# Performance work log

Hardware: AMD Instinct MI355X
Metric: run time of the kernel (lower is better)

The kernel has to match this reference:

```python
import jax, jax.numpy as jnp
import numpy as np

N_NODES = 100000
N_EDGES = 1600000
DIM = 64
NEG_SLOPE = 0.2  # DGL GATConv default
BN_EPS = 1e-5


def setup_inputs() -> dict:
    key = jax.random.key(0)
    ks = jax.random.split(key, 16)
    d = {}
    d["node_weight"] = jax.random.normal(ks[0], (N_NODES, DIM), jnp.float32)
    d["edge_weight"] = jax.random.normal(ks[1], (N_EDGES,), jnp.float32)  # unused in forward (faithful to source)
    d["src"] = jax.random.randint(ks[2], (N_EDGES,), 0, N_NODES)
    d["dst"] = jax.random.randint(ks[3], (N_EDGES,), 0, N_NODES)
    i = 4
    scale = 1.0 / np.sqrt(DIM)
    for l in (1, 2, 3):
        d[f"W{l}"] = jax.random.normal(ks[i], (DIM, DIM), jnp.float32) * scale; i += 1
        d[f"al{l}"] = jax.random.normal(ks[i], (DIM,), jnp.float32) * 0.1; i += 1
        d[f"ar{l}"] = jax.random.normal(ks[i], (DIM,), jnp.float32) * 0.1; i += 1
        d[f"b{l}"] = jnp.zeros((DIM,), jnp.float32)
        d[f"g{l}"] = jnp.ones((DIM,), jnp.float32)
        d[f"beta{l}"] = jnp.zeros((DIM,), jnp.float32)
    return d


def gat_layer(h, src, dst, W, al, ar, b):
    # DGL GATConv, 1 head: project, edge attention, per-dst softmax, scatter-add
    feat = h @ W                                  # [N, D]
    el = feat @ al                                # [N]
    er = feat @ ar                                # [N]
    e = jax.nn.leaky_relu(el[src] + er[dst], NEG_SLOPE)   # [E]
    m = jax.ops.segment_max(e, dst, num_segments=N_NODES)  # per-dst max
    ex = jnp.exp(e - m[dst])
    s = jax.ops.segment_sum(ex, dst, num_segments=N_NODES)
    alpha = ex / s[dst]                           # edge softmax
    out = jax.ops.segment_sum(alpha[:, None] * feat[src], dst, num_segments=N_NODES)
    return out + b


def batchnorm(h, g, beta):
    # BatchNorm1d in training mode: batch stats, biased variance
    mu = jnp.mean(h, axis=0)
    var = jnp.mean(jnp.square(h - mu), axis=0)
    return (h - mu) * jax.lax.rsqrt(var + BN_EPS) * g + beta


def reference(node_weight, edge_weight, src, dst,
              W1, al1, ar1, b1, g1, beta1,
              W2, al2, ar2, b2, g2, beta2,
              W3, al3, ar3, b3, g3, beta3):
    # dropout is identity in eval mode
    h = gat_layer(node_weight, src, dst, W1, al1, ar1, b1)
    h = jax.nn.elu(batchnorm(h, g1, beta1))
    h = gat_layer(h, src, dst, W2, al2, ar2, b2)
    h = jax.nn.elu(batchnorm(h, g2, beta2))
    h = gat_layer(h, src, dst, W3, al3, ar3, b3)
    h = batchnorm(h, g3, beta3)
    return h
```

## Files before the change

kernel.cpp:

```cpp
#include <hip/hip_runtime.h>
#include <hip/hip_bf16.h>
#include <math.h>

#define DIM 64
#define BSHIFT 9
#define BNODES 512
#define MAXB 256
#define EPT 8
#define CHUNK 2048

typedef __attribute__((ext_vector_type(8))) short bf16x8;
typedef __attribute__((ext_vector_type(4))) float f32x4;

__device__ __forceinline__ short f2bf(float x) {
    union { __hip_bfloat16 b; short s; } u;
    u.b = __float2bfloat16(x);
    return u.s;
}
__device__ __forceinline__ float bf2f(short s) {
    return __uint_as_float(((unsigned)(unsigned short)s) << 16);
}


__global__ void bin_count_kernel(const int* __restrict__ dst, int* __restrict__ bucket_cnt, int E) {
    __shared__ int h[MAXB];
    int t = threadIdx.x;
    h[t] = 0;
    __syncthreads();
    for (int i = blockIdx.x * blockDim.x + t; i < E; i += gridDim.x * blockDim.x)
        atomicAdd(&h[dst[i] >> BSHIFT], 1);
    __syncthreads();
    if (h[t]) atomicAdd(&bucket_cnt[t], h[t]);
}

__global__ void bucket_scan_kernel(const int* __restrict__ bucket_cnt,
                                   int* __restrict__ bucket_off, int* __restrict__ bucket_fill) {
    __shared__ int s[MAXB];
    int t = threadIdx.x;
    int v = bucket_cnt[t];
    s[t] = v;
    __syncthreads();
    for (int off = 1; off < MAXB; off <<= 1) {
        int x = (t >= off) ? s[t - off] : 0;
        __syncthreads();
        s[t] += x;
        __syncthreads();
    }
    bucket_off[t] = s[t] - v;
    bucket_fill[t] = 0;
}

__global__ __launch_bounds__(256) void bin_scatter_kernel(
    const int* __restrict__ src, const int* __restrict__ dst,
    const int* __restrict__ bucket_off, int* __restrict__ bucket_fill,
    unsigned long long* __restrict__ binned, int E) {
    __shared__ int lcnt[MAXB];
    __shared__ int lbase[MAXB];
    int t = threadIdx.x;
    lcnt[t] = 0;
    __syncthreads();
    int base = blockIdx.x * CHUNK;
    unsigned long long pair[EPT];
    int slot[EPT];
#pragma unroll
    for (int j = 0; j < EPT; j++) {
        int idx = base + j * 256 + t;
        if (idx < E) {
            int s = src[idx], d = dst[idx];
            pair[j] = ((unsigned long long)(unsigned)d << 32) | (unsigned)s;
            slot[j] = atomicAdd(&lcnt[d >> BSHIFT], 1);
        } else {
            slot[j] = -1;
        }
    }
    __syncthreads();
    int c = lcnt[t];
    if (c) lbase[t] = atomicAdd(&bucket_fill[t], c);
    __syncthreads();
#pragma unroll
    for (int j = 0; j < EPT; j++) {
        if (slot[j] >= 0) {
            int b = (int)(pair[j] >> 32) >> BSHIFT;
            binned[(size_t)bucket_off[b] + lbase[b] + slot[j]] = pair[j];
        }
    }
}

__global__ __launch_bounds__(256) void node_count_kernel(
    const unsigned long long* __restrict__ binned, const int* __restrict__ bucket_off,
    const int* __restrict__ bucket_cnt, int* __restrict__ counts, int N) {
    __shared__ int cnt[BNODES];
    int b = blockIdx.x, t = threadIdx.x;
    for (int i = t; i < BNODES; i += 256) cnt[i] = 0;
    __syncthreads();
    int s0 = bucket_off[b], c = bucket_cnt[b];
    for (int i = t; i < c; i += 256) {
        int d = (int)(binned[(size_t)s0 + i] >> 32);
        atomicAdd(&cnt[d & (BNODES - 1)], 1);
    }
    __syncthreads();
    int nbase = b << BSHIFT;
    for (int i = t; i < BNODES; i += 256)
        if (nbase + i < N) counts[nbase + i] = cnt[i];
}

__global__ void scan1_kernel(const int* __restrict__ counts, int* __restrict__ excl,
                             int* __restrict__ blk_sums, int n) {
    __shared__ int sdata[256];
    int t = threadIdx.x;
    int base = blockIdx.x * 1024 + t * 4;
    int v0 = (base + 0 < n) ? counts[base + 0] : 0;
    int v1 = (base + 1 < n) ? counts[base + 1] : 0;
    int v2 = (base + 2 < n) ? counts[base + 2] : 0;
    int v3 = (base + 3 < n) ? counts[base + 3] : 0;
    int tsum = v0 + v1 + v2 + v3;
    sdata[t] = tsum;
    __syncthreads();
    for (int off = 1; off < 256; off <<= 1) {
        int x = (t >= off) ? sdata[t - off] : 0;
        __syncthreads();
        sdata[t] += x;
        __syncthreads();
    }
    int run = sdata[t] - tsum;
    if (base + 0 < n) excl[base + 0] = run; run += v0;
    if (base + 1 < n) excl[base + 1] = run; run += v1;
    if (base + 2 < n) excl[base + 2] = run; run += v2;
    if (base + 3 < n) excl[base + 3] = run;
    if (t == 255) blk_sums[blockIdx.x] = sdata[255];
}

__global__ void scan2_kernel(int* __restrict__ blk_sums, int nb) {
    __shared__ int s[128];
    int t = threadIdx.x;
    s[t] = (t < nb) ? blk_sums[t] : 0;
    __syncthreads();
    for (int off = 1; off < 128; off <<= 1) {
        int x = (t >= off) ? s[t - off] : 0;
        __syncthreads();
        s[t] += x;
        __syncthreads();
    }
    if (t < nb) blk_sums[t] = (t > 0) ? s[t - 1] : 0;
}

__global__ void scan3_kernel(int* __restrict__ excl, const int* __restrict__ blk_sums,
                             int n, int total) {
    int i = blockIdx.x * blockDim.x + threadIdx.x;
    if (i < n) excl[i] += blk_sums[i >> 10];
    if (i == 0) excl[n] = total;
}

__global__ __launch_bounds__(256) void final_scatter_kernel(
    const unsigned long long* __restrict__ binned, const int* __restrict__ bucket_off,
    const int* __restrict__ bucket_cnt, const int* __restrict__ row_ptr,
    int* __restrict__ src_sorted, int N) {
    __shared__ int fill[BNODES];
    int b = blockIdx.x, t = threadIdx.x;
    for (int i = t; i < BNODES; i += 256) fill[i] = 0;
    __syncthreads();
    int s0 = bucket_off[b], c = bucket_cnt[b];
    for (int i = t; i < c; i += 256) {
        unsigned long long p = binned[(size_t)s0 + i];
        int d = (int)(p >> 32);
        int pos = row_ptr[d] + atomicAdd(&fill[d & (BNODES - 1)], 1);
        src_sorted[pos] = (int)(p & 0xffffffffu);
    }
}


__global__ void wlr_kernel(
    const float* __restrict__ W1, const float* __restrict__ al1, const float* __restrict__ ar1,
    const float* __restrict__ W2, const float* __restrict__ al2, const float* __restrict__ ar2,
    const float* __restrict__ W3, const float* __restrict__ al3, const float* __restrict__ ar3,
    float* __restrict__ wlr, short* __restrict__ wfrag) {
    const float* W  = (blockIdx.x == 0) ? W1  : (blockIdx.x == 1) ? W2  : W3;
    const float* al = (blockIdx.x == 0) ? al1 : (blockIdx.x == 1) ? al2 : al3;
    const float* ar = (blockIdx.x == 0) ? ar1 : (blockIdx.x == 1) ? ar2 : ar3;
    int t = threadIdx.x;
    short* whi = wfrag + blockIdx.x * 8192;
    short* wlo = whi + 4096;
    for (int idx = t; idx < 4096; idx += 256) {
        int j = idx & 7, li = (idx >> 3) & 15, quad = (idx >> 7) & 3;
        int nt = (idx >> 9) & 3, ks = idx >> 11;
        int k = ks * 32 + quad * 8 + j, nn = nt * 16 + li;
        float w = W[k * 64 + nn];
        short hi = f2bf(w);
        whi[idx] = hi;
        wlo[idx] = f2bf(w - bf2f(hi));
    }
    if (t < 64) {
        float l = 0.f, r = 0.f;
        for (int nn = 0; nn < 64; nn++) {
            float w = W[t * 64 + nn];
            l = fmaf(w, al[nn], l);
            r = fmaf(w, ar[nn], r);
        }
        const float LOG2E = 1.4426950408889634f;
        wlr[blockIdx.x * 128 + t] = l * LOG2E;
        wlr[blockIdx.x * 128 + 64 + t] = r * LOG2E;
    }
}

__global__ __launch_bounds__(256) void gemm64_mfma_kernel(
    const float* __restrict__ h, const short* __restrict__ wfrag_l,
    const float* __restrict__ wl, const float* __restrict__ wr,
    const float* __restrict__ stats, const float* __restrict__ g,
    const float* __restrict__ beta, int do_bn, float invN,
    __hip_bfloat16* __restrict__ feat, float* __restrict__ el, float* __restrict__ er,
    int n) {
    int t = threadIdx.x;
    int lane = t & 63;
    int li = lane & 15;
    int quad = lane >> 4;
    int wv = t >> 6;

    const short* whi = wfrag_l;
    const short* wlo = wfrag_l + 4096;
    bf16x8 b_hi[2][4], b_lo[2][4];
#pragma unroll
    for (int ks = 0; ks < 2; ks++)
#pragma unroll
        for (int nt = 0; nt < 4; nt++) {
            int base = (((ks * 4 + nt) * 4 + quad) * 16 + li) * 8;
            b_hi[ks][nt] = *(const bf16x8*)(whi + base);
            b_lo[ks][nt] = *(const bf16x8*)(wlo + base);
        }
    float wlv[2][8], wrv[2][8];
#pragma unroll
    for (int ks = 0; ks < 2; ks++)
#pragma unroll
        for (int j = 0; j < 8; j++) {
            wlv[ks][j] = wl[ks * 32 + quad * 8 + j];
            wrv[ks][j] = wr[ks * 32 + quad * 8 + j];
        }

    float sc[2][8], sh[2][8];
    if (do_bn) {
#pragma unroll
        for (int ks = 0; ks < 2; ks++)
#pragma unroll
            for (int j = 0; j < 8; j++) {
                int k = ks * 32 + quad * 8 + j;
                float mu = stats[k] * invN;
                float var = fmaf(-mu, mu, stats[64 + k] * invN);
                float inv = rsqrtf(var + 1e-5f) * g[k];
                sc[ks][j] = inv;
                sh[ks][j] = beta[k] - mu * inv;
            }
    }

    int ntiles = (n + 15) >> 4;
    for (int tile = blockIdx.x * 4 + wv; tile < ntiles; tile += gridDim.x * 4) {
        int m0 = tile << 4;
        int rrow = m0 + li;
        const float* rowp = h + (size_t)((rrow < n) ? rrow : (n - 1)) * 64;
        bf16x8 a_hi[2], a_lo[2];
        float elp = 0.f, erp = 0.f;
#pragma unroll
        for (int ks = 0; ks < 2; ks++) {
            float4 v0 = *(const float4*)(rowp + ks * 32 + quad * 8);
            float4 v1 = *(const float4*)(rowp + ks * 32 + quad * 8 + 4);
            float x[8] = {v0.x, v0.y, v0.z, v0.w, v1.x, v1.y, v1.z, v1.w};
#pragma unroll
            for (int j = 0; j < 8; j++) {
                float v = x[j];
                if (do_bn) {
                    v = fmaf(v, sc[ks][j], sh[ks][j]);
                    if (v < 0.f) v = expm1f(v);
                }
                elp = fmaf(v, wlv[ks][j], elp);
                erp = fmaf(v, wrv[ks][j], erp);
                short hi = f2bf(v);
                a_hi[ks][j] = hi;
                a_lo[ks][j] = f2bf(v - bf2f(hi));
            }
        }
        elp += __shfl_xor(elp, 16, 64);
        elp += __shfl_xor(elp, 32, 64);
        erp += __shfl_xor(erp, 16, 64);
        erp += __shfl_xor(erp, 32, 64);
        if (lane < 16 && m0 + li < n) {
            el[m0 + li] = elp;
            er[m0 + li] = erp;
        }
        f32x4 acc[4];
#pragma unroll
        for (int nt = 0; nt < 4; nt++) acc[nt] = (f32x4){0.f, 0.f, 0.f, 0.f};
#pragma unroll
        for (int ks = 0; ks < 2; ks++)
#pragma unroll
            for (int nt = 0; nt < 4; nt++) {
                acc[nt] = __builtin_amdgcn_mfma_f32_16x16x32_bf16(a_hi[ks], b_hi[ks][nt], acc[nt], 0, 0, 0);
                acc[nt] = __builtin_amdgcn_mfma_f32_16x16x32_bf16(a_lo[ks], b_hi[ks][nt], acc[nt], 0, 0, 0);
                acc[nt] = __builtin_amdgcn_mfma_f32_16x16x32_bf16(a_hi[ks], b_lo[ks][nt], acc[nt], 0, 0, 0);
            }
#pragma unroll
        for (int nt = 0; nt < 4; nt++)
#pragma unroll
            for (int reg = 0; reg < 4; reg++) {
                int wrow = m0 + quad * 4 + reg;
                if (wrow < n) {
                    union { __hip_bfloat16 b; short s; } u;
                    u.s = f2bf(acc[nt][reg]);
                    feat[(size_t)wrow * 64 + nt * 16 + li] = u.b;
                }
            }
    }
}

#define AGG_LOAD(P, ELV, POS)                                  \
    {                                                          \
        int idx = (POS) + q;                                   \
        bool v = idx < end;                                    \
        int idc = v ? idx : end - 1;                           \
        int sn = src_sorted[idc];                              \
        float ev = el[sn];                                     \
        ELV = v ? ev : -INFINITY;                              \
        P = featv[(size_t)sn * 8 + li];                        \
    }

#define AGG_CHUNK(P, ELV)                                      \
    {                                                          \
        float e = ELV + er_n;                                  \
        e = fmaxf(e, 0.2f * e);                                \
        float w = exp2f(e);                                    \
        s += w;                                                \
        a0 = fmaf(w, __uint_as_float(P.x << 16), a0);          \
        a1 = fmaf(w, __uint_as_float(P.x & 0xffff0000u), a1);  \
        a2 = fmaf(w, __uint_as_float(P.y << 16), a2);          \
        a3 = fmaf(w, __uint_as_float(P.y & 0xffff0000u), a3);  \
        a4 = fmaf(w, __uint_as_float(P.z << 16), a4);          \
        a5 = fmaf(w, __uint_as_float(P.z & 0xffff0000u), a5);  \
        a6 = fmaf(w, __uint_as_float(P.w << 16), a6);          \
        a7 = fmaf(w, __uint_as_float(P.w & 0xffff0000u), a7);  \
    }

__global__ __launch_bounds__(256) void attn_agg_kernel(
    const int* __restrict__ row_ptr, const int* __restrict__ src_sorted,
    const float* __restrict__ el, const float* __restrict__ er,
    const __hip_bfloat16* __restrict__ feat, const float* __restrict__ bias,
    float* __restrict__ out, int n) {
    int t = threadIdx.x, lane = t & 63;
    int q = lane >> 3;
    int li = lane & 7;
    int node0 = blockIdx.x * 16 + (t >> 6) * 4;
    const uint4* featv = (const uint4*)feat;

#pragma unroll
    for (int j = 0; j < 4; j++) {
        int node = node0 + j;
        if (node >= n) break;
        int start = row_ptr[node], end = row_ptr[node + 1];
        float er_n = er[node];

        float s = 0.f;
        float a0 = 0.f, a1 = 0.f, a2 = 0.f, a3 = 0.f;
        float a4 = 0.f, a5 = 0.f, a6 = 0.f, a7 = 0.f;

        uint4 pA = {0u, 0u, 0u, 0u}, pB = {0u, 0u, 0u, 0u};
        float elA = -INFINITY, elB = -INFINITY;
        if (start < end) AGG_LOAD(pA, elA, start)
        if (start + 8 < end) AGG_LOAD(pB, elB, start + 8)
        for (int i = start; i < end; i += 16) {
            AGG_CHUNK(pA, elA)
            if (i + 16 < end) AGG_LOAD(pA, elA, i + 16)
            if (i + 8 < end) {
                AGG_CHUNK(pB, elB)
                if (i + 24 < end) AGG_LOAD(pB, elB, i + 24)
            }
        }
        s += __shfl_xor(s, 8, 64);
        s += __shfl_xor(s, 16, 64);
        s += __shfl_xor(s, 32, 64);
        bool b0 = (q & 1) != 0;
        float t0 = __shfl_xor(a0, 8, 64), t1 = __shfl_xor(a1, 8, 64);
        float t2 = __shfl_xor(a2, 8, 64), t3 = __shfl_xor(a3, 8, 64);
        float t4 = __shfl_xor(a4, 8, 64), t5 = __shfl_xor(a5, 8, 64);
        float t6 = __shfl_xor(a6, 8, 64), t7 = __shfl_xor(a7, 8, 64);
        float x0 = b0 ? (a4 + t4) : (a0 + t0);
        float x1 = b0 ? (a5 + t5) : (a1 + t1);
        float y0 = b0 ? (a6 + t6) : (a2 + t2);
        float y1 = b0 ? (a7 + t7) : (a3 + t3);
        bool b1 = (q & 2) != 0;
        float u0 = __shfl_xor(x0, 16, 64), u1 = __shfl_xor(x1, 16, 64);
        float v0 = __shfl_xor(y0, 16, 64), v1 = __shfl_xor(y1, 16, 64);
        float z0 = b1 ? (y0 + v0) : (x0 + u0);
        float z1 = b1 ? (y1 + v1) : (x1 + u1);
        z0 += __shfl_xor(z0, 32, 64);
        z1 += __shfl_xor(z1, 32, 64);
        float val = ((q & 4) != 0) ? z1 : z0;
        int d = li * 8 + ((q & 1) << 2) + (q & 2) + ((q >> 2) & 1);
        float inv_s = (s > 0.f) ? 1.f / s : 0.f;
        out[(size_t)node * 64 + d] = fmaf(val, inv_s, bias[d]);
    }
}

__global__ __launch_bounds__(256) void bn_stats_kernel(const float* __restrict__ h,
                                                       float* __restrict__ stats, int n) {
    __shared__ float ls[256], lss[256];
    int t = threadIdx.x, lane = t & 63;
    int w = blockIdx.x * 4 + (t >> 6);
    int stride = gridDim.x * 4;
    float s = 0.f, ss = 0.f;
    for (int row = w; row < n; row += stride) {
        float v = h[(size_t)row * DIM + lane];
        s += v;
        ss = fmaf(v, v, ss);
    }
    ls[t] = s; lss[t] = ss;
    __syncthreads();
    if (t < 64) {
        float a = ls[t] + ls[t + 64] + ls[t + 128] + ls[t + 192];
        float b = lss[t] + lss[t + 64] + lss[t + 128] + lss[t + 192];
        atomicAdd(&stats[t], a);
        atomicAdd(&stats[64 + t], b);
    }
}

__global__ void bn_apply_kernel(float* __restrict__ h, const float* __restrict__ stats,
                                const float* __restrict__ g, const float* __restrict__ beta,
                                int n, int do_elu) {
    int i = blockIdx.x * blockDim.x + threadIdx.x;
    int total = n * DIM;
    int stride = gridDim.x * blockDim.x;
    float invN = 1.f / (float)n;
    for (; i < total; i += stride) {
        int c = i & 63;
        float mu = stats[c] * invN;
        float var = fmaf(-mu, mu, stats[DIM + c] * invN);
        float x = (h[i] - mu) * rsqrtf(var + 1e-5f) * g[c] + beta[c];
        if (do_elu && x < 0.f) x = expm1f(x);
        h[i] = x;
    }
}


extern "C" void kernel_launch(void* const* d_in, const int* in_sizes, int n_in,
                              void* d_out, int out_size, void* d_ws, size_t ws_size,
                              hipStream_t stream) {
    const float* nw = (const float*)d_in[0];
    const int* src = (const int*)d_in[2];
    const int* dst = (const int*)d_in[3];
    const int N = in_sizes[0] / DIM;
    const int E = in_sizes[2];
    const float invN = 1.f / (float)N;
    const int nbuck = (N + BNODES - 1) >> BSHIFT;

    char* ws = (char*)d_ws;
    size_t off = 0;
    auto alloc = [&](size_t bytes) -> void* {
        void* p = ws + off;
        off += (bytes + 255) & ~(size_t)255;
        return p;
    };
    int* counts       = (int*)alloc((size_t)N * 4);
    int* row_ptr      = (int*)alloc(((size_t)N + 1) * 4);
    int* blk_sums     = (int*)alloc(512);
    int* bucket_cnt   = (int*)alloc(MAXB * 4);
    int* bucket_off   = (int*)alloc(MAXB * 4);
    int* bucket_fill  = (int*)alloc(MAXB * 4);
    unsigned long long* binned = (unsigned long long*)alloc((size_t)E * 8);
    int* src_sorted   = (int*)alloc((size_t)E * 4);
    float* el         = (float*)alloc((size_t)N * 4);
    float* er         = (float*)alloc((size_t)N * 4);
    __hip_bfloat16* feat = (__hip_bfloat16*)alloc((size_t)N * DIM * 2);
    float* hbuf       = (float*)alloc((size_t)N * DIM * 4);
    float* stats      = (float*)alloc(3 * 512);
    float* wlr        = (float*)alloc(3 * 128 * 4);
    short* wfrag      = (short*)alloc(3 * 8192 * 2);

    int nb = (N + 1023) / 1024;
    int ntiles = (N + 15) >> 4;

    hipMemsetAsync(bucket_cnt, 0, MAXB * 4, stream);
    hipMemsetAsync(stats, 0, 3 * 512, stream);
    wlr_kernel<<<3, 256, 0, stream>>>(
        (const float*)d_in[4],  (const float*)d_in[5],  (const float*)d_in[6],
        (const float*)d_in[10], (const float*)d_in[11], (const float*)d_in[12],
        (const float*)d_in[16], (const float*)d_in[17], (const float*)d_in[18],
        wlr, wfrag);
    bin_count_kernel<<<256, 256, 0, stream>>>(dst, bucket_cnt, E);
    bucket_scan_kernel<<<1, MAXB, 0, stream>>>(bucket_cnt, bucket_off, bucket_fill);
    bin_scatter_kernel<<<(E + CHUNK - 1) / CHUNK, 256, 0, stream>>>(
        src, dst, bucket_off, bucket_fill, binned, E);
    node_count_kernel<<<nbuck, 256, 0, stream>>>(binned, bucket_off, bucket_cnt, counts, N);
    scan1_kernel<<<nb, 256, 0, stream>>>(counts, row_ptr, blk_sums, N);
    scan2_kernel<<<1, 128, 0, stream>>>(blk_sums, nb);
    scan3_kernel<<<(N + 255) / 256, 256, 0, stream>>>(row_ptr, blk_sums, N, E);
    final_scatter_kernel<<<nbuck, 256, 0, stream>>>(binned, bucket_off, bucket_cnt,
                                                    row_ptr, src_sorted, N);

    for (int l = 0; l < 3; l++) {
        const float* b    = (const float*)d_in[7 + 6 * l];
        const float* hin = (l == 0) ? nw : hbuf;
        float* hout = (l == 2) ? (float*)d_out : hbuf;
        float* stats_prev = (l == 0) ? stats : stats + (l - 1) * 128;
        float* stats_cur  = stats + l * 128;

        gemm64_mfma_kernel<<<(ntiles + 3) / 4, 256, 0, stream>>>(
            hin, wfrag + l * 8192,
            wlr + l * 128, wlr + l * 128 + 64,
            stats_prev,
            (l == 0) ? (const float*)d_in[8] : (const float*)d_in[8 + 6 * (l - 1)],
            (l == 0) ? (const float*)d_in[9] : (const float*)d_in[9 + 6 * (l - 1)],
            (l > 0) ? 1 : 0, invN,
            feat, el, er, N);
        attn_agg_kernel<<<(N + 15) / 16, 256, 0, stream>>>(row_ptr, src_sorted, el, er,
                                                           feat, b, hout, N);
        bn_stats_kernel<<<512, 256, 0, stream>>>(hout, stats_cur, N);
    }
    bn_apply_kernel<<<2048, 256, 0, stream>>>((float*)d_out, stats + 2 * 128,
                                              (const float*)d_in[8 + 12],
                                              (const float*)d_in[9 + 12],
                                              N, 0);
}
```

Measured before the change: 474.0 us.

## Replace two-level bucketed CSR build with direct global-atomic count and scatter

Replaces the bucket-binning CSR construction (bin count, bucket scan, bin scatter, per-bucket node count, final scatter) with a single global-atomic per-node count kernel and a single global-atomic scatter kernel. This cuts several kernel launches and the intermediate 8-byte binned edge array pass. In exchange it relies on 1.6M global atomics spread over 100K counters and on scattered writes, where the old scheme used LDS atomics and bucket-local writes. Edge order within each destination row also becomes nondeterministic.

```diff
diff --git a/kernel.cpp b/kernel.cpp
--- a/kernel.cpp
+++ b/kernel.cpp
@@ -3,11 +3,6 @@
 #include <math.h>
 
 #define DIM 64
-#define BSHIFT 9
-#define BNODES 512
-#define MAXB 256
-#define EPT 8
-#define CHUNK 2048
 
 typedef __attribute__((ext_vector_type(8))) short bf16x8;
 typedef __attribute__((ext_vector_type(4))) float f32x4;
@@ -22,86 +17,25 @@
 }
 
 
-__global__ void bin_count_kernel(const int* __restrict__ dst, int* __restrict__ bucket_cnt, int E) {
-    __shared__ int h[MAXB];
-    int t = threadIdx.x;
-    h[t] = 0;
-    __syncthreads();
-    for (int i = blockIdx.x * blockDim.x + t; i < E; i += gridDim.x * blockDim.x)
-        atomicAdd(&h[dst[i] >> BSHIFT], 1);
-    __syncthreads();
-    if (h[t]) atomicAdd(&bucket_cnt[t], h[t]);
-}
-
-__global__ void bucket_scan_kernel(const int* __restrict__ bucket_cnt,
-                                   int* __restrict__ bucket_off, int* __restrict__ bucket_fill) {
-    __shared__ int s[MAXB];
-    int t = threadIdx.x;
-    int v = bucket_cnt[t];
-    s[t] = v;
-    __syncthreads();
-    for (int off = 1; off < MAXB; off <<= 1) {
-        int x = (t >= off) ? s[t - off] : 0;
-        __syncthreads();
-        s[t] += x;
-        __syncthreads();
-    }
-    bucket_off[t] = s[t] - v;
-    bucket_fill[t] = 0;
-}
-
-__global__ __launch_bounds__(256) void bin_scatter_kernel(
+__global__ __launch_bounds__(256) void count_kernel(
+    const int* __restrict__ dst, int* __restrict__ counts, int E) {
+    int i = blockIdx.x * blockDim.x + threadIdx.x;
+    int stride = gridDim.x * blockDim.x;
+    for (; i < E; i += stride)
+        atomicAdd(&counts[dst[i]], 1);
+}
+
+__global__ __launch_bounds__(256) void scatter_kernel(
     const int* __restrict__ src, const int* __restrict__ dst,
-    const int* __restrict__ bucket_off, int* __restrict__ bucket_fill,
-    unsigned long long* __restrict__ binned, int E) {
-    __shared__ int lcnt[MAXB];
-    __shared__ int lbase[MAXB];
-    int t = threadIdx.x;
-    lcnt[t] = 0;
-    __syncthreads();
-    int base = blockIdx.x * CHUNK;
-    unsigned long long pair[EPT];
-    int slot[EPT];
-#pragma unroll
-    for (int j = 0; j < EPT; j++) {
-        int idx = base + j * 256 + t;
-        if (idx < E) {
-            int s = src[idx], d = dst[idx];
-            pair[j] = ((unsigned long long)(unsigned)d << 32) | (unsigned)s;
-            slot[j] = atomicAdd(&lcnt[d >> BSHIFT], 1);
-        } else {
-            slot[j] = -1;
-        }
-    }
-    __syncthreads();
-    int c = lcnt[t];
-    if (c) lbase[t] = atomicAdd(&bucket_fill[t], c);
-    __syncthreads();
-#pragma unroll
-    for (int j = 0; j < EPT; j++) {
-        if (slot[j] >= 0) {
-            int b = (int)(pair[j] >> 32) >> BSHIFT;
-            binned[(size_t)bucket_off[b] + lbase[b] + slot[j]] = pair[j];
-        }
-    }
-}
-
-__global__ __launch_bounds__(256) void node_count_kernel(
-    const unsigned long long* __restrict__ binned, const int* __restrict__ bucket_off,
-    const int* __restrict__ bucket_cnt, int* __restrict__ counts, int N) {
-    __shared__ int cnt[BNODES];
-    int b = blockIdx.x, t = threadIdx.x;
-    for (int i = t; i < BNODES; i += 256) cnt[i] = 0;
-    __syncthreads();
-    int s0 = bucket_off[b], c = bucket_cnt[b];
-    for (int i = t; i < c; i += 256) {
-        int d = (int)(binned[(size_t)s0 + i] >> 32);
-        atomicAdd(&cnt[d & (BNODES - 1)], 1);
-    }
-    __syncthreads();
-    int nbase = b << BSHIFT;
-    for (int i = t; i < BNODES; i += 256)
-        if (nbase + i < N) counts[nbase + i] = cnt[i];
+    const int* __restrict__ row_ptr, int* __restrict__ fill,
+    int* __restrict__ src_sorted, int E) {
+    int i = blockIdx.x * blockDim.x + threadIdx.x;
+    int stride = gridDim.x * blockDim.x;
+    for (; i < E; i += stride) {
+        int d = dst[i];
+        int pos = row_ptr[d] + atomicAdd(&fill[d], 1);
+        src_sorted[pos] = src[i];
+    }
 }
 
 __global__ void scan1_kernel(const int* __restrict__ counts, int* __restrict__ excl,
@@ -149,23 +83,6 @@
     int i = blockIdx.x * blockDim.x + threadIdx.x;
     if (i < n) excl[i] += blk_sums[i >> 10];
     if (i == 0) excl[n] = total;
-}
-
-__global__ __launch_bounds__(256) void final_scatter_kernel(
-    const unsigned long long* __restrict__ binned, const int* __restrict__ bucket_off,
-    const int* __restrict__ bucket_cnt, const int* __restrict__ row_ptr,
-    int* __restrict__ src_sorted, int N) {
-    __shared__ int fill[BNODES];
-    int b = blockIdx.x, t = threadIdx.x;
-    for (int i = t; i < BNODES; i += 256) fill[i] = 0;
-    __syncthreads();
-    int s0 = bucket_off[b], c = bucket_cnt[b];
-    for (int i = t; i < c; i += 256) {
-        unsigned long long p = binned[(size_t)s0 + i];
-        int d = (int)(p >> 32);
-        int pos = row_ptr[d] + atomicAdd(&fill[d & (BNODES - 1)], 1);
-        src_sorted[pos] = (int)(p & 0xffffffffu);
-    }
 }
 
 
@@ -445,7 +362,6 @@
     const int N = in_sizes[0] / DIM;
     const int E = in_sizes[2];
     const float invN = 1.f / (float)N;
-    const int nbuck = (N + BNODES - 1) >> BSHIFT;
 
     char* ws = (char*)d_ws;
     size_t off = 0;
@@ -454,13 +370,10 @@
         off += (bytes + 255) & ~(size_t)255;
         return p;
     };
-    int* counts       = (int*)alloc((size_t)N * 4);
+    int* counts       = (int*)alloc((size_t)N * 2 * 4);
+    int* fill         = counts + N;
     int* row_ptr      = (int*)alloc(((size_t)N + 1) * 4);
     int* blk_sums     = (int*)alloc(512);
-    int* bucket_cnt   = (int*)alloc(MAXB * 4);
-    int* bucket_off   = (int*)alloc(MAXB * 4);
-    int* bucket_fill  = (int*)alloc(MAXB * 4);
-    unsigned long long* binned = (unsigned long long*)alloc((size_t)E * 8);
     int* src_sorted   = (int*)alloc((size_t)E * 4);
     float* el         = (float*)alloc((size_t)N * 4);
     float* er         = (float*)alloc((size_t)N * 4);
@@ -473,23 +386,18 @@
     int nb = (N + 1023) / 1024;
     int ntiles = (N + 15) >> 4;
 
-    hipMemsetAsync(bucket_cnt, 0, MAXB * 4, stream);
+    hipMemsetAsync(counts, 0, (size_t)N * 2 * 4, stream);
     hipMemsetAsync(stats, 0, 3 * 512, stream);
     wlr_kernel<<<3, 256, 0, stream>>>(
         (const float*)d_in[4],  (const float*)d_in[5],  (const float*)d_in[6],
         (const float*)d_in[10], (const float*)d_in[11], (const float*)d_in[12],
         (const float*)d_in[16], (const float*)d_in[17], (const float*)d_in[18],
         wlr, wfrag);
-    bin_count_kernel<<<256, 256, 0, stream>>>(dst, bucket_cnt, E);
-    bucket_scan_kernel<<<1, MAXB, 0, stream>>>(bucket_cnt, bucket_off, bucket_fill);
-    bin_scatter_kernel<<<(E + CHUNK - 1) / CHUNK, 256, 0, stream>>>(
-        src, dst, bucket_off, bucket_fill, binned, E);
-    node_count_kernel<<<nbuck, 256, 0, stream>>>(binned, bucket_off, bucket_cnt, counts, N);
+    count_kernel<<<2048, 256, 0, stream>>>(dst, counts, E);
     scan1_kernel<<<nb, 256, 0, stream>>>(counts, row_ptr, blk_sums, N);
     scan2_kernel<<<1, 128, 0, stream>>>(blk_sums, nb);
     scan3_kernel<<<(N + 255) / 256, 256, 0, stream>>>(row_ptr, blk_sums, N, E);
-    final_scatter_kernel<<<nbuck, 256, 0, stream>>>(binned, bucket_off, bucket_cnt,
-                                                    row_ptr, src_sorted, N);
+    scatter_kernel<<<2048, 256, 0, stream>>>(src, dst, row_ptr, fill, src_sorted, E);
 
     for (int l = 0; l < 3; l++) {
         const float* b    = (const float*)d_in[7 + 6 * l];
```

Result: slower. 567.7 us (+19.8%).

## Fuse CSR build into one per-bucket kernel and store hidden activations in bf16

Applied to the files above, without the earlier changes.

Replaces the node-count, three-stage global scan and final scatter kernels with a single per-bucket kernel. It computes local counts, does a shared-memory exclusive scan offset by the bucket base, writes row_ptr and scatters src indices, which removes four launches and the counts round-trip. Intermediate layer outputs (hbuf) are now stored as bf16 instead of fp32, halving the write traffic in attn_agg and the read traffic in bn_stats and the next GEMM. The cost is lower precision for intermediate activations before batchnorm statistics.

```diff
diff --git a/kernel.cpp b/kernel.cpp
--- a/kernel.cpp
+++ b/kernel.cpp
@@ -86,85 +86,45 @@
     }
 }
 
-__global__ __launch_bounds__(256) void node_count_kernel(
+__global__ __launch_bounds__(256) void csr_finalize_kernel(
     const unsigned long long* __restrict__ binned, const int* __restrict__ bucket_off,
-    const int* __restrict__ bucket_cnt, int* __restrict__ counts, int N) {
+    const int* __restrict__ bucket_cnt, int* __restrict__ row_ptr,
+    int* __restrict__ src_sorted, int N, int E, int nbuck) {
     __shared__ int cnt[BNODES];
+    __shared__ int excl[BNODES];
+    __shared__ int ps[256];
     int b = blockIdx.x, t = threadIdx.x;
     for (int i = t; i < BNODES; i += 256) cnt[i] = 0;
     __syncthreads();
     int s0 = bucket_off[b], c = bucket_cnt[b];
-    for (int i = t; i < c; i += 256) {
-        int d = (int)(binned[(size_t)s0 + i] >> 32);
-        atomicAdd(&cnt[d & (BNODES - 1)], 1);
-    }
+    for (int i = t; i < c; i += 256)
+        atomicAdd(&cnt[(int)(binned[(size_t)s0 + i] >> 32) & (BNODES - 1)], 1);
+    __syncthreads();
+    int a0 = cnt[2 * t], a1 = cnt[2 * t + 1];
+    int pairsum = a0 + a1;
+    ps[t] = pairsum;
+    __syncthreads();
+    for (int off = 1; off < 256; off <<= 1) {
+        int x = (t >= off) ? ps[t - off] : 0;
+        __syncthreads();
+        ps[t] += x;
+        __syncthreads();
+    }
+    int run = ps[t] - pairsum;
+    excl[2 * t] = run;
+    excl[2 * t + 1] = run + a0;
     __syncthreads();
     int nbase = b << BSHIFT;
     for (int i = t; i < BNODES; i += 256)
-        if (nbase + i < N) counts[nbase + i] = cnt[i];
-}
-
-__global__ void scan1_kernel(const int* __restrict__ counts, int* __restrict__ excl,
-                             int* __restrict__ blk_sums, int n) {
-    __shared__ int sdata[256];
-    int t = threadIdx.x;
-    int base = blockIdx.x * 1024 + t * 4;
-    int v0 = (base + 0 < n) ? counts[base + 0] : 0;
-    int v1 = (base + 1 < n) ? counts[base + 1] : 0;
-    int v2 = (base + 2 < n) ? counts[base + 2] : 0;
-    int v3 = (base + 3 < n) ? counts[base + 3] : 0;
-    int tsum = v0 + v1 + v2 + v3;
-    sdata[t] = tsum;
-    __syncthreads();
-    for (int off = 1; off < 256; off <<= 1) {
-        int x = (t >= off) ? sdata[t - off] : 0;
-        __syncthreads();
-        sdata[t] += x;
-        __syncthreads();
-    }
-    int run = sdata[t] - tsum;
-    if (base + 0 < n) excl[base + 0] = run; run += v0;
-    if (base + 1 < n) excl[base + 1] = run; run += v1;
-    if (base + 2 < n) excl[base + 2] = run; run += v2;
-    if (base + 3 < n) excl[base + 3] = run;
-    if (t == 255) blk_sums[blockIdx.x] = sdata[255];
-}
-
-__global__ void scan2_kernel(int* __restrict__ blk_sums, int nb) {
-    __shared__ int s[128];
-    int t = threadIdx.x;
-    s[t] = (t < nb) ? blk_sums[t] : 0;
-    __syncthreads();
-    for (int off = 1; off < 128; off <<= 1) {
-        int x = (t >= off) ? s[t - off] : 0;
-        __syncthreads();
-        s[t] += x;
-        __syncthreads();
-    }
-    if (t < nb) blk_sums[t] = (t > 0) ? s[t - 1] : 0;
-}
-
-__global__ void scan3_kernel(int* __restrict__ excl, const int* __restrict__ blk_sums,
-                             int n, int total) {
-    int i = blockIdx.x * blockDim.x + threadIdx.x;
-    if (i < n) excl[i] += blk_sums[i >> 10];
-    if (i == 0) excl[n] = total;
-}
-
-__global__ __launch_bounds__(256) void final_scatter_kernel(
-    const unsigned long long* __restrict__ binned, const int* __restrict__ bucket_off,
-    const int* __restrict__ bucket_cnt, const int* __restrict__ row_ptr,
-    int* __restrict__ src_sorted, int N) {
-    __shared__ int fill[BNODES];
-    int b = blockIdx.x, t = threadIdx.x;
-    for (int i = t; i < BNODES; i += 256) fill[i] = 0;
-    __syncthreads();
-    int s0 = bucket_off[b], c = bucket_cnt[b];
+        if (nbase + i < N) row_ptr[nbase + i] = s0 + excl[i];
+    if (b == nbuck - 1 && t == 0) row_ptr[N] = E;
+    for (int i = t; i < BNODES; i += 256) cnt[i] = 0;
+    __syncthreads();
     for (int i = t; i < c; i += 256) {
         unsigned long long p = binned[(size_t)s0 + i];
-        int d = (int)(p >> 32);
-        int pos = row_ptr[d] + atomicAdd(&fill[d & (BNODES - 1)], 1);
-        src_sorted[pos] = (int)(p & 0xffffffffu);
+        int d = (int)(p >> 32) & (BNODES - 1);
+        int pos = excl[d] + atomicAdd(&cnt[d], 1);
+        src_sorted[(size_t)s0 + pos] = (int)(p & 0xffffffffu);
     }
 }
 
@@ -203,7 +163,7 @@
 }
 
 __global__ __launch_bounds__(256) void gemm64_mfma_kernel(
-    const float* __restrict__ h, const short* __restrict__ wfrag_l,
+    const void* __restrict__ hvoid, int in_bf16, const short* __restrict__ wfrag_l,
     const float* __restrict__ wl, const float* __restrict__ wr,
     const float* __restrict__ stats, const float* __restrict__ g,
     const float* __restrict__ beta, int do_bn, float invN,
@@ -254,14 +214,26 @@
     for (int tile = blockIdx.x * 4 + wv; tile < ntiles; tile += gridDim.x * 4) {
         int m0 = tile << 4;
         int rrow = m0 + li;
-        const float* rowp = h + (size_t)((rrow < n) ? rrow : (n - 1)) * 64;
+        size_t rowbase = (size_t)((rrow < n) ? rrow : (n - 1)) * 64;
         bf16x8 a_hi[2], a_lo[2];
         float elp = 0.f, erp = 0.f;
 #pragma unroll
         for (int ks = 0; ks < 2; ks++) {
-            float4 v0 = *(const float4*)(rowp + ks * 32 + quad * 8);
-            float4 v1 = *(const float4*)(rowp + ks * 32 + quad * 8 + 4);
-            float x[8] = {v0.x, v0.y, v0.z, v0.w, v1.x, v1.y, v1.z, v1.w};
+            float x[8];
+            if (in_bf16) {
+                const unsigned short* rp = (const unsigned short*)hvoid + rowbase + ks * 32 + quad * 8;
+                uint4 pv = *(const uint4*)rp;
+                x[0] = bf2f((short)(pv.x & 0xffffu)); x[1] = bf2f((short)(pv.x >> 16));
+                x[2] = bf2f((short)(pv.y & 0xffffu)); x[3] = bf2f((short)(pv.y >> 16));
+                x[4] = bf2f((short)(pv.z & 0xffffu)); x[5] = bf2f((short)(pv.z >> 16));
+                x[6] = bf2f((short)(pv.w & 0xffffu)); x[7] = bf2f((short)(pv.w >> 16));
+            } else {
+                const float* rp = (const float*)hvoid + rowbase + ks * 32 + quad * 8;
+                float4 v0 = *(const float4*)rp;
+                float4 v1 = *(const float4*)(rp + 4);
+                x[0] = v0.x; x[1] = v0.y; x[2] = v0.z; x[3] = v0.w;
+                x[4] = v1.x; x[5] = v1.y; x[6] = v1.z; x[7] = v1.w;
+            }
 #pragma unroll
             for (int j = 0; j < 8; j++) {
                 float v = x[j];
@@ -340,10 +312,12 @@
     const int* __restrict__ row_ptr, const int* __restrict__ src_sorted,
     const float* __restrict__ el, const float* __restrict__ er,
     const __hip_bfloat16* __restrict__ feat, const float* __restrict__ bias,
-    float* __restrict__ out, int n) {
+    void* __restrict__ outv, int out_bf16, int n) {
     int t = threadIdx.x, lane = t & 63;
     int q = lane >> 3;
     int li = lane & 7;
+    int d = li * 8 + ((q & 1) << 2) + (q & 2) + ((q >> 2) & 1);
+    float bias_d = bias[d];
     int node0 = blockIdx.x * 16 + (t >> 6) * 4;
     const uint4* featv = (const uint4*)feat;
 
@@ -390,13 +364,20 @@
         z0 += __shfl_xor(z0, 32, 64);
         z1 += __shfl_xor(z1, 32, 64);
         float val = ((q & 4) != 0) ? z1 : z0;
-        int d = li * 8 + ((q & 1) << 2) + (q & 2) + ((q >> 2) & 1);
         float inv_s = (s > 0.f) ? 1.f / s : 0.f;
-        out[(size_t)node * 64 + d] = fmaf(val, inv_s, bias[d]);
-    }
-}
-
-__global__ __launch_bounds__(256) void bn_stats_kernel(const float* __restrict__ h,
+        float x = fmaf(val, inv_s, bias_d);
+        if (out_bf16) {
+            union { __hip_bfloat16 b; short s2; } u;
+            u.s2 = f2bf(x);
+            ((__hip_bfloat16*)outv)[(size_t)node * 64 + d] = u.b;
+        } else {
+            ((float*)outv)[(size_t)node * 64 + d] = x;
+        }
+    }
+}
+
+__global__ __launch_bounds__(256) void bn_stats_kernel(const void* __restrict__ hvoid,
+                                                       int in_bf16,
                                                        float* __restrict__ stats, int n) {
     __shared__ float ls[256], lss[256];
     int t = threadIdx.x, lane = t & 63;
@@ -404,7 +385,9 @@
     int stride = gridDim.x * 4;
     float s = 0.f, ss = 0.f;
     for (int row = w; row < n; row += stride) {
-        float v = h[(size_t)row * DIM + lane];
+        float v;
+        if (in_bf16) v = bf2f((short)((const unsigned short*)hvoid)[(size_t)row * DIM + lane]);
+        else         v = ((const float*)hvoid)[(size_t)row * DIM + lane];
         s += v;
         ss = fmaf(v, v, ss);
     }
@@ -454,9 +437,7 @@
         off += (bytes + 255) & ~(size_t)255;
         return p;
     };
-    int* counts       = (int*)alloc((size_t)N * 4);
     int* row_ptr      = (int*)alloc(((size_t)N + 1) * 4);
-    int* blk_sums     = (int*)alloc(512);
     int* bucket_cnt   = (int*)alloc(MAXB * 4);
     int* bucket_off   = (int*)alloc(MAXB * 4);
     int* bucket_fill  = (int*)alloc(MAXB * 4);
@@ -465,12 +446,11 @@
     float* el         = (float*)alloc((size_t)N * 4);
     float* er         = (float*)alloc((size_t)N * 4);
     __hip_bfloat16* feat = (__hip_bfloat16*)alloc((size_t)N * DIM * 2);
-    float* hbuf       = (float*)alloc((size_t)N * DIM * 4);
+    __hip_bfloat16* hbuf = (__hip_bfloat16*)alloc((size_t)N * DIM * 2);
     float* stats      = (float*)alloc(3 * 512);
     float* wlr        = (float*)alloc(3 * 128 * 4);
     short* wfrag      = (short*)alloc(3 * 8192 * 2);
 
-    int nb = (N + 1023) / 1024;
     int ntiles = (N + 15) >> 4;
 
     hipMemsetAsync(bucket_cnt, 0, MAXB * 4, stream);
@@ -484,22 +464,20 @@
     bucket_scan_kernel<<<1, MAXB, 0, stream>>>(bucket_cnt, bucket_off, bucket_fill);
     bin_scatter_kernel<<<(E + CHUNK - 1) / CHUNK, 256, 0, stream>>>(
         src, dst, bucket_off, bucket_fill, binned, E);
-    node_count_kernel<<<nbuck, 256, 0, stream>>>(binned, bucket_off, bucket_cnt, counts, N);
-    scan1_kernel<<<nb, 256, 0, stream>>>(counts, row_ptr, blk_sums, N);
-    scan2_kernel<<<1, 128, 0, stream>>>(blk_sums, nb);
-    scan3_kernel<<<(N + 255) / 256, 256, 0, stream>>>(row_ptr, blk_sums, N, E);
-    final_scatter_kernel<<<nbuck, 256, 0, stream>>>(binned, bucket_off, bucket_cnt,
-                                                    row_ptr, src_sorted, N);
+    csr_finalize_kernel<<<nbuck, 256, 0, stream>>>(binned, bucket_off, bucket_cnt,
+                                                   row_ptr, src_sorted, N, E, nbuck);
 
     for (int l = 0; l < 3; l++) {
         const float* b    = (const float*)d_in[7 + 6 * l];
-        const float* hin = (l == 0) ? nw : hbuf;
-        float* hout = (l == 2) ? (float*)d_out : hbuf;
+        const void* hin   = (l == 0) ? (const void*)nw : (const void*)hbuf;
+        int in_bf16       = (l == 0) ? 0 : 1;
+        void* hout        = (l == 2) ? (void*)d_out : (void*)hbuf;
+        int out_bf16      = (l == 2) ? 0 : 1;
         float* stats_prev = (l == 0) ? stats : stats + (l - 1) * 128;
         float* stats_cur  = stats + l * 128;
 
         gemm64_mfma_kernel<<<(ntiles + 3) / 4, 256, 0, stream>>>(
-            hin, wfrag + l * 8192,
+            hin, in_bf16, wfrag + l * 8192,
             wlr + l * 128, wlr + l * 128 + 64,
             stats_prev,
             (l == 0) ? (const float*)d_in[8] : (const float*)d_in[8 + 6 * (l - 1)],
@@ -507,8 +485,8 @@
             (l > 0) ? 1 : 0, invN,
             feat, el, er, N);
         attn_agg_kernel<<<(N + 15) / 16, 256, 0, stream>>>(row_ptr, src_sorted, el, er,
-                                                           feat, b, hout, N);
-        bn_stats_kernel<<<512, 256, 0, stream>>>(hout, stats_cur, N);
+                                                           feat, b, hout, out_bf16, N);
+        bn_stats_kernel<<<512, 256, 0, stream>>>(hout, out_bf16, stats_cur, N);
     }
     bn_apply_kernel<<<2048, 256, 0, stream>>>((float*)d_out, stats + 2 * 128,
                                               (const float*)d_in[8 + 12],
```

Measured after the change: 463.0 us. -2.3%, faster.
